# Optimization experiments

Measured on AMD Instinct MI355X. Metric: run time of the kernel, lower is better.

## Reference

```python
import jax
import jax.numpy as jnp
from jax import lax
import numpy as np

INPUT_DIM = 784
HIDDEN_DIM = 1024
BATCH = 256
N_BINS = 10


def setup_inputs() -> dict:
    key = jax.random.key(0)
    k1, k2, k3, k4, k5 = jax.random.split(key, 5)
    # kaiming-normal-ish init scales (faithful in spirit; exact values irrelevant for math)
    W = jax.random.normal(k1, (HIDDEN_DIM, INPUT_DIM), dtype=jnp.float32) * np.sqrt(2.0 / INPUT_DIM)
    c = jnp.zeros((HIDDEN_DIM, 1), dtype=jnp.float32)
    V = jax.random.normal(k2, (INPUT_DIM, HIDDEN_DIM, N_BINS), dtype=jnp.float32) * np.sqrt(2.0 / N_BINS)
    b = jnp.zeros((INPUT_DIM, N_BINS), dtype=jnp.float32)
    x = jax.random.randint(k3, (BATCH, INPUT_DIM), 0, N_BINS, dtype=jnp.int32)
    return {"x": x, "W": W, "c": c, "V": V, "b": b}


def reference(x, W, c, V, b):
    # x: [B, D] int pixel bins; W: [H, D]; c: [H, 1]; V: [D, H, 10]; b: [D, 10]
    B = x.shape[0]
    xf = x.astype(jnp.float32)  # [B, D]
    a0 = jnp.broadcast_to(c[:, 0][None, :], (B, W.shape[0]))  # [B, H]

    def step(a, inp):
        Vi, bi, Wi, xi = inp  # Vi:[H,10], bi:[10], Wi:[H], xi:[B]
        h = jax.nn.sigmoid(a)                       # [B, H]
        p = jax.nn.softmax(h @ Vi + bi, axis=1)     # [B, 10]
        a = a + xi[:, None] * Wi[None, :]           # rank-1 update, matches x_i @ W[:,i].T
        return a, p

    _, p_seq = lax.scan(step, a0, (V, b, W.T, xf.T))  # p_seq: [D, B, 10]
    p_hat = jnp.transpose(p_seq, (1, 2, 0))            # [B, 10, D] == torch.stack(p_hat, dim=2)
    return p_hat
```

## Files before the change

kernel.cpp:

```cpp
#include <hip/hip_runtime.h>
#include <stdint.h>

#define D_DIM 784
#define H_DIM 1024
#define B_DIM 256
#define NBIN  10
#define G_CH  8
#define T_CH  98
#define BT    16
#define BF    2
#define LOG2E 1.4426950408889634f

typedef _Float16 half8_t  __attribute__((ext_vector_type(8)));
typedef __fp16   fp16x2_t __attribute__((ext_vector_type(2)));
typedef float    float4_t __attribute__((ext_vector_type(4)));

__global__ void k_transpose(const float* __restrict__ W, float* __restrict__ Wt2) {
    __shared__ float t[64][65];
    int j0 = blockIdx.x * 64, h0 = blockIdx.y * 64;
    int tj = threadIdx.x & 63, tr = threadIdx.x >> 6;
    int j = j0 + tj;
    #pragma unroll
    for (int r = 0; r < 16; ++r) {
        int hh = tr * 16 + r;
        t[hh][tj] = (j < D_DIM) ? W[(size_t)(h0 + hh) * D_DIM + j] : 0.0f;
    }
    __syncthreads();
    #pragma unroll
    for (int r = 0; r < 16; ++r) {
        int jj = tr * 16 + r;
        int jo = j0 + jj;
        if (jo < D_DIM) Wt2[(size_t)jo * H_DIM + h0 + tj] = t[tj][jj] * LOG2E;
    }
}

__global__ void k_vbprep(const float* __restrict__ V, _Float16* __restrict__ VB) {
    int i   = blockIdx.x;
    int tid = threadIdx.x;
    __shared__ __align__(16) float vsf[H_DIM * NBIN];
    const float4* src = (const float4*)(V + (size_t)i * H_DIM * NBIN);
    #pragma unroll
    for (int q = 0; q < 10; ++q) {
        float4 v = src[q * 256 + tid];
        *((float4*)&vsf[(q * 256 + tid) * 4]) = v;
    }
    __syncthreads();
    #pragma unroll
    for (int q = 0; q < 8; ++q) {
        int pair = q * 256 + tid;
        int kk = pair >> 6, l = pair & 63;
        int n = l & 15, hb = kk * 32 + ((l >> 4) & 3) * 8;
        union { _Float16 h[8]; uint4 u; } o;
        #pragma unroll
        for (int jj = 0; jj < 8; ++jj)
            o.h[jj] = (_Float16)((n < NBIN) ? vsf[(hb + jj) * NBIN + n] : 0.0f);
        ((uint4*)VB)[(size_t)i * 2048 + pair] = o.u;
    }
}

__global__ void k_pscan(const float* __restrict__ Wt2, const int* __restrict__ x,
                        const float* __restrict__ c, _Float16* __restrict__ PA) {
    int b0 = blockIdx.x * BF;
    int h  = blockIdx.y * 256 + threadIdx.x;
    __shared__ float xs[BF][D_DIM];
    for (int q = threadIdx.x; q < BF * (D_DIM / 4); q += 256) {
        int bb = q / (D_DIM / 4), r = q % (D_DIM / 4);
        int4 xi = ((const int4*)(x + (size_t)(b0 + bb) * D_DIM))[r];
        float4 xf = make_float4((float)xi.x, (float)xi.y, (float)xi.z, (float)xi.w);
        *((float4*)&xs[bb][r * 4]) = xf;
    }
    float acc0 = c[h] * LOG2E, acc1 = acc0;
    __syncthreads();
    for (int t = 0; t < T_CH; ++t) {
        PA[((size_t)t * B_DIM + b0 + 0) * H_DIM + h] = (_Float16)acc0;
        PA[((size_t)t * B_DIM + b0 + 1) * H_DIM + h] = (_Float16)acc1;
        #pragma unroll
        for (int j = 0; j < G_CH; ++j) {
            float wv = Wt2[(size_t)(t * G_CH + j) * H_DIM + h];
            acc0 += xs[0][t * G_CH + j] * wv;
            acc1 += xs[1][t * G_CH + j] * wv;
        }
    }
}

__global__ __launch_bounds__(256, 2)
void k_main(const float* __restrict__ Wt2, const _Float16* __restrict__ VB,
            const _Float16* __restrict__ PA, const int* __restrict__ x,
            const float* __restrict__ bias, float* __restrict__ out) {
    int bt  = blockIdx.x;
    int tc  = blockIdx.y;
    int tid = threadIdx.x;
    int w   = tid >> 6;
    int l   = tid & 63;
    int bl  = l & 15;
    int kg  = l >> 4;
    int bg  = bt * BT + bl;
    int i0  = tc * G_CH;

    __shared__ __align__(16) _Float16 wlds[G_CH][H_DIM];
    __shared__ float red[2][4][64][5];
    __shared__ float bs[G_CH][16];
    __shared__ __align__(16) float plds[BT][NBIN][12];

    {
        int ii = tid >> 4, n = tid & 15;
        if (ii < G_CH) bs[ii][n] = (n < NBIN) ? bias[(size_t)(i0 + ii) * NBIN + n] : 0.0f;
    }
    {
        #pragma unroll
        for (int r = 0; r < G_CH; ++r) {
            float4 v = ((const float4*)(Wt2 + (size_t)(i0 + r) * H_DIM))[tid];
            union { fp16x2_t v2[2]; uint2 u; } cv;
            cv.v2[0] = __builtin_amdgcn_cvt_pkrtz(v.x, v.y);
            cv.v2[1] = __builtin_amdgcn_cvt_pkrtz(v.z, v.w);
            *((uint2*)&wlds[r][tid * 4]) = cv.u;
        }
    }
    float xvf[G_CH];
    {
        const int4* xp = (const int4*)(x + (size_t)bg * D_DIM + i0);
        int4 x0 = xp[0], x1 = xp[1];
        xvf[0] = (float)x0.x; xvf[1] = (float)x0.y; xvf[2] = (float)x0.z; xvf[3] = (float)x0.w;
        xvf[4] = (float)x1.x; xvf[5] = (float)x1.y; xvf[6] = (float)x1.z; xvf[7] = (float)x1.w;
    }
    float a[8][8];
    {
        const _Float16* src = PA + ((size_t)tc * B_DIM + bg) * H_DIM + w * 256 + kg * 8;
        #pragma unroll
        for (int m = 0; m < 8; ++m) {
            half8_t av = *((const half8_t*)(src + m * 32));
            #pragma unroll
            for (int j = 0; j < 8; ++j) a[m][j] = (float)av[j];
        }
    }
    __syncthreads();

    const uint4* vbbase = (const uint4*)VB;
    #pragma unroll 1
    for (int ii = 0; ii < G_CH; ++ii) {
        int i = i0 + ii;
        int par = ii & 1;

        uint4 vb[8];
        const uint4* vbp = vbbase + ((size_t)i * 32 + w * 8) * 64 + l;
        #pragma unroll
        for (int m = 0; m < 8; ++m) vb[m] = vbp[m * 64];

        if (ii > 0) {
            int ip = ii - 1, pp = par ^ 1;
            float tot = red[pp][0][l][w] + red[pp][1][l][w] + red[pp][2][l][w] + red[pp][3][l][w];
            int n = bl;
            float v = (n < NBIN) ? tot + bs[ip][n] : -3.0e38f;
            float vm = v;
            vm = fmaxf(vm, __shfl_xor(vm, 1));
            vm = fmaxf(vm, __shfl_xor(vm, 2));
            vm = fmaxf(vm, __shfl_xor(vm, 4));
            vm = fmaxf(vm, __shfl_xor(vm, 8));
            float e = __builtin_amdgcn_exp2f((v - vm) * LOG2E);
            float ss = e;
            ss += __shfl_xor(ss, 1); ss += __shfl_xor(ss, 2);
            ss += __shfl_xor(ss, 4); ss += __shfl_xor(ss, 8);
            float p = e * __builtin_amdgcn_rcpf(ss);
            if (n < NBIN) plds[kg * 4 + w][n][ip] = p;
        }

        float xf = xvf[ii];
        float4_t cfrag = {0.f, 0.f, 0.f, 0.f};
        #pragma unroll
        for (int m = 0; m < 8; ++m) {
            union { half8_t h8; uint u32[4]; } af;
            #pragma unroll
            for (int p = 0; p < 4; ++p) {
                float s0 = __builtin_amdgcn_rcpf(1.0f + __builtin_amdgcn_exp2f(-a[m][2 * p]));
                float s1 = __builtin_amdgcn_rcpf(1.0f + __builtin_amdgcn_exp2f(-a[m][2 * p + 1]));
                union { fp16x2_t v; uint u; } cv;
                cv.v = __builtin_amdgcn_cvt_pkrtz(s0, s1);
                af.u32[p] = cv.u;
            }
            union { half8_t h8; uint4 u; } bf;
            bf.u = vb[m];
            cfrag = __builtin_amdgcn_mfma_f32_16x16x32_f16(af.h8, bf.h8, cfrag, 0, 0, 0);

            half8_t wh = *((const half8_t*)&wlds[ii][w * 256 + kg * 8 + m * 32]);
            a[m][0] += xf * (float)wh[0]; a[m][1] += xf * (float)wh[1];
            a[m][2] += xf * (float)wh[2]; a[m][3] += xf * (float)wh[3];
            a[m][4] += xf * (float)wh[4]; a[m][5] += xf * (float)wh[5];
            a[m][6] += xf * (float)wh[6]; a[m][7] += xf * (float)wh[7];
        }

        red[par][w][l][0] = cfrag[0]; red[par][w][l][1] = cfrag[1];
        red[par][w][l][2] = cfrag[2]; red[par][w][l][3] = cfrag[3];
        __syncthreads();
    }
    {
        int ip = G_CH - 1, pp = (G_CH - 1) & 1;
        float tot = red[pp][0][l][w] + red[pp][1][l][w] + red[pp][2][l][w] + red[pp][3][l][w];
        int n = bl;
        float v = (n < NBIN) ? tot + bs[ip][n] : -3.0e38f;
        float vm = v;
        vm = fmaxf(vm, __shfl_xor(vm, 1));
        vm = fmaxf(vm, __shfl_xor(vm, 2));
        vm = fmaxf(vm, __shfl_xor(vm, 4));
        vm = fmaxf(vm, __shfl_xor(vm, 8));
        float e = __builtin_amdgcn_exp2f((v - vm) * LOG2E);
        float ss = e;
        ss += __shfl_xor(ss, 1); ss += __shfl_xor(ss, 2);
        ss += __shfl_xor(ss, 4); ss += __shfl_xor(ss, 8);
        float p = e * __builtin_amdgcn_rcpf(ss);
        if (n < NBIN) plds[kg * 4 + w][n][ip] = p;
    }
    __syncthreads();

    if (tid < BT * NBIN) {
        int bb = tid / NBIN, n = tid % NBIN;
        size_t base = ((size_t)(bt * BT + bb) * NBIN + n) * D_DIM + i0;
        #pragma unroll
        for (int q = 0; q < 2; ++q) {
            float4 v = *((float4*)&plds[bb][n][q * 4]);
            *((float4*)(out + base + q * 4)) = v;
        }
    }
}

extern "C" void kernel_launch(void* const* d_in, const int* in_sizes, int n_in,
                              void* d_out, int out_size, void* d_ws, size_t ws_size,
                              hipStream_t stream) {
    const int*   x    = (const int*)d_in[0];
    const float* W    = (const float*)d_in[1];
    const float* c    = (const float*)d_in[2];
    const float* V    = (const float*)d_in[3];
    const float* bias = (const float*)d_in[4];
    float* out = (float*)d_out;

    char* ws = (char*)d_ws;
    size_t off = 0;
    float* Wt2 = (float*)(ws + off);
    off += (size_t)D_DIM * H_DIM * sizeof(float);
    off = (off + 255) & ~(size_t)255;
    _Float16* VB = (_Float16*)(ws + off);
    off += (size_t)D_DIM * 32 * 64 * 8 * sizeof(_Float16);
    off = (off + 255) & ~(size_t)255;
    _Float16* PA = (_Float16*)(ws + off);

    k_transpose<<<dim3(13, 16), 256, 0, stream>>>(W, Wt2);
    k_vbprep<<<dim3(D_DIM), 256, 0, stream>>>(V, VB);
    k_pscan<<<dim3(B_DIM / BF, 4), 256, 0, stream>>>(Wt2, x, c, PA);
    k_main<<<dim3(B_DIM / BT, T_CH), 256, 0, stream>>>(Wt2, VB, PA, x, bias, out);
}
```

Measured before the change: 202.1 us.

## Merge prep kernels, store transposed W in fp16, batch softmax reductions in main

Fuses the W transpose and V reformat into one launch with a block-index split, and stores the scaled transposed W as fp16, which halves its traffic in pscan and main and removes the conversion in main. In the main kernel, per-step barriers and softmax are replaced by computing four pixel steps at a time, staging all four MFMA fragments into a wider LDS buffer, and doing softmax plus a direct float4 global store twice per block instead of eight times through a staging array. This cuts barriers from eight to four and removes the final output-staging pass. The cost is more live registers for the held fragments and lower-precision W in the prefix scan, whose errors accumulate across 784 steps.

```diff
diff --git a/kernel.cpp b/kernel.cpp
--- a/kernel.cpp
+++ b/kernel.cpp
@@ -15,50 +15,52 @@
 typedef __fp16   fp16x2_t __attribute__((ext_vector_type(2)));
 typedef float    float4_t __attribute__((ext_vector_type(4)));
 
-__global__ void k_transpose(const float* __restrict__ W, float* __restrict__ Wt2) {
-    __shared__ float t[64][65];
-    int j0 = blockIdx.x * 64, h0 = blockIdx.y * 64;
-    int tj = threadIdx.x & 63, tr = threadIdx.x >> 6;
-    int j = j0 + tj;
-    #pragma unroll
-    for (int r = 0; r < 16; ++r) {
-        int hh = tr * 16 + r;
-        t[hh][tj] = (j < D_DIM) ? W[(size_t)(h0 + hh) * D_DIM + j] : 0.0f;
-    }
-    __syncthreads();
-    #pragma unroll
-    for (int r = 0; r < 16; ++r) {
-        int jj = tr * 16 + r;
-        int jo = j0 + jj;
-        if (jo < D_DIM) Wt2[(size_t)jo * H_DIM + h0 + tj] = t[tj][jj] * LOG2E;
-    }
-}
-
-__global__ void k_vbprep(const float* __restrict__ V, _Float16* __restrict__ VB) {
-    int i   = blockIdx.x;
+__global__ void k_prep(const float* __restrict__ W, const float* __restrict__ V,
+                       _Float16* __restrict__ Wt2h, _Float16* __restrict__ VB) {
+    __shared__ __align__(16) float smem[H_DIM * NBIN];
     int tid = threadIdx.x;
-    __shared__ __align__(16) float vsf[H_DIM * NBIN];
-    const float4* src = (const float4*)(V + (size_t)i * H_DIM * NBIN);
-    #pragma unroll
-    for (int q = 0; q < 10; ++q) {
-        float4 v = src[q * 256 + tid];
-        *((float4*)&vsf[(q * 256 + tid) * 4]) = v;
-    }
-    __syncthreads();
-    #pragma unroll
-    for (int q = 0; q < 8; ++q) {
-        int pair = q * 256 + tid;
-        int kk = pair >> 6, l = pair & 63;
-        int n = l & 15, hb = kk * 32 + ((l >> 4) & 3) * 8;
-        union { _Float16 h[8]; uint4 u; } o;
-        #pragma unroll
-        for (int jj = 0; jj < 8; ++jj)
-            o.h[jj] = (_Float16)((n < NBIN) ? vsf[(hb + jj) * NBIN + n] : 0.0f);
-        ((uint4*)VB)[(size_t)i * 2048 + pair] = o.u;
-    }
-}
-
-__global__ void k_pscan(const float* __restrict__ Wt2, const int* __restrict__ x,
+    if (blockIdx.x < D_DIM) {
+        int i = blockIdx.x;
+        const float4* src = (const float4*)(V + (size_t)i * H_DIM * NBIN);
+        #pragma unroll
+        for (int q = 0; q < 10; ++q) {
+            float4 v = src[q * 256 + tid];
+            *((float4*)&smem[(q * 256 + tid) * 4]) = v;
+        }
+        __syncthreads();
+        #pragma unroll
+        for (int q = 0; q < 8; ++q) {
+            int pair = q * 256 + tid;
+            int kk = pair >> 6, l = pair & 63;
+            int n = l & 15, hb = kk * 32 + ((l >> 4) & 3) * 8;
+            union { _Float16 h[8]; uint4 u; } o;
+            #pragma unroll
+            for (int jj = 0; jj < 8; ++jj)
+                o.h[jj] = (_Float16)((n < NBIN) ? smem[(hb + jj) * NBIN + n] : 0.0f);
+            ((uint4*)VB)[(size_t)i * 2048 + pair] = o.u;
+        }
+    } else {
+        int q = blockIdx.x - D_DIM;
+        int j0 = (q % 13) * 64, h0 = (q / 13) * 64;
+        float (*t)[65] = (float(*)[65])smem;
+        int tj = tid & 63, tr = tid >> 6;
+        int j = j0 + tj;
+        #pragma unroll
+        for (int r = 0; r < 16; ++r) {
+            int hh = tr * 16 + r;
+            t[hh][tj] = (j < D_DIM) ? W[(size_t)(h0 + hh) * D_DIM + j] : 0.0f;
+        }
+        __syncthreads();
+        #pragma unroll
+        for (int r = 0; r < 16; ++r) {
+            int jj = tr * 16 + r;
+            int jo = j0 + jj;
+            if (jo < D_DIM) Wt2h[(size_t)jo * H_DIM + h0 + tj] = (_Float16)(t[tj][jj] * LOG2E);
+        }
+    }
+}
+
+__global__ void k_pscan(const _Float16* __restrict__ Wt2h, const int* __restrict__ x,
                         const float* __restrict__ c, _Float16* __restrict__ PA) {
     int b0 = blockIdx.x * BF;
     int h  = blockIdx.y * 256 + threadIdx.x;
@@ -76,7 +78,7 @@
         PA[((size_t)t * B_DIM + b0 + 1) * H_DIM + h] = (_Float16)acc1;
         #pragma unroll
         for (int j = 0; j < G_CH; ++j) {
-            float wv = Wt2[(size_t)(t * G_CH + j) * H_DIM + h];
+            float wv = (float)Wt2h[(size_t)(t * G_CH + j) * H_DIM + h];
             acc0 += xs[0][t * G_CH + j] * wv;
             acc1 += xs[1][t * G_CH + j] * wv;
         }
@@ -84,7 +86,7 @@
 }
 
 __global__ __launch_bounds__(256, 2)
-void k_main(const float* __restrict__ Wt2, const _Float16* __restrict__ VB,
+void k_main(const _Float16* __restrict__ VB, const _Float16* __restrict__ Wt2h,
             const _Float16* __restrict__ PA, const int* __restrict__ x,
             const float* __restrict__ bias, float* __restrict__ out) {
     int bt  = blockIdx.x;
@@ -98,9 +100,8 @@
     int i0  = tc * G_CH;
 
     __shared__ __align__(16) _Float16 wlds[G_CH][H_DIM];
-    __shared__ float red[2][4][64][5];
+    __shared__ float red[4][64][18];
     __shared__ float bs[G_CH][16];
-    __shared__ __align__(16) float plds[BT][NBIN][12];
 
     {
         int ii = tid >> 4, n = tid & 15;
@@ -109,11 +110,8 @@
     {
         #pragma unroll
         for (int r = 0; r < G_CH; ++r) {
-            float4 v = ((const float4*)(Wt2 + (size_t)(i0 + r) * H_DIM))[tid];
-            union { fp16x2_t v2[2]; uint2 u; } cv;
-            cv.v2[0] = __builtin_amdgcn_cvt_pkrtz(v.x, v.y);
-            cv.v2[1] = __builtin_amdgcn_cvt_pkrtz(v.z, v.w);
-            *((uint2*)&wlds[r][tid * 4]) = cv.u;
+            uint2 v = ((const uint2*)(Wt2h + (size_t)(i0 + r) * H_DIM))[tid];
+            *((uint2*)&wlds[r][tid * 4]) = v;
         }
     }
     float xvf[G_CH];
@@ -136,36 +134,16 @@
     __syncthreads();
 
     const uint4* vbbase = (const uint4*)VB;
-    #pragma unroll 1
-    for (int ii = 0; ii < G_CH; ++ii) {
+    float4_t cf[G_CH];
+
+    auto compute_ii = [&](int ii) {
         int i = i0 + ii;
-        int par = ii & 1;
-
         uint4 vb[8];
         const uint4* vbp = vbbase + ((size_t)i * 32 + w * 8) * 64 + l;
         #pragma unroll
         for (int m = 0; m < 8; ++m) vb[m] = vbp[m * 64];
-
-        if (ii > 0) {
-            int ip = ii - 1, pp = par ^ 1;
-            float tot = red[pp][0][l][w] + red[pp][1][l][w] + red[pp][2][l][w] + red[pp][3][l][w];
-            int n = bl;
-            float v = (n < NBIN) ? tot + bs[ip][n] : -3.0e38f;
-            float vm = v;
-            vm = fmaxf(vm, __shfl_xor(vm, 1));
-            vm = fmaxf(vm, __shfl_xor(vm, 2));
-            vm = fmaxf(vm, __shfl_xor(vm, 4));
-            vm = fmaxf(vm, __shfl_xor(vm, 8));
-            float e = __builtin_amdgcn_exp2f((v - vm) * LOG2E);
-            float ss = e;
-            ss += __shfl_xor(ss, 1); ss += __shfl_xor(ss, 2);
-            ss += __shfl_xor(ss, 4); ss += __shfl_xor(ss, 8);
-            float p = e * __builtin_amdgcn_rcpf(ss);
-            if (n < NBIN) plds[kg * 4 + w][n][ip] = p;
-        }
-
         float xf = xvf[ii];
-        float4_t cfrag = {0.f, 0.f, 0.f, 0.f};
+        float4_t cfr = {0.f, 0.f, 0.f, 0.f};
         #pragma unroll
         for (int m = 0; m < 8; ++m) {
             union { half8_t h8; uint u32[4]; } af;
@@ -179,47 +157,60 @@
             }
             union { half8_t h8; uint4 u; } bf;
             bf.u = vb[m];
-            cfrag = __builtin_amdgcn_mfma_f32_16x16x32_f16(af.h8, bf.h8, cfrag, 0, 0, 0);
-
+            cfr = __builtin_amdgcn_mfma_f32_16x16x32_f16(af.h8, bf.h8, cfr, 0, 0, 0);
             half8_t wh = *((const half8_t*)&wlds[ii][w * 256 + kg * 8 + m * 32]);
             a[m][0] += xf * (float)wh[0]; a[m][1] += xf * (float)wh[1];
             a[m][2] += xf * (float)wh[2]; a[m][3] += xf * (float)wh[3];
             a[m][4] += xf * (float)wh[4]; a[m][5] += xf * (float)wh[5];
             a[m][6] += xf * (float)wh[6]; a[m][7] += xf * (float)wh[7];
         }
-
-        red[par][w][l][0] = cfrag[0]; red[par][w][l][1] = cfrag[1];
-        red[par][w][l][2] = cfrag[2]; red[par][w][l][3] = cfrag[3];
-        __syncthreads();
-    }
-    {
-        int ip = G_CH - 1, pp = (G_CH - 1) & 1;
-        float tot = red[pp][0][l][w] + red[pp][1][l][w] + red[pp][2][l][w] + red[pp][3][l][w];
-        int n = bl;
-        float v = (n < NBIN) ? tot + bs[ip][n] : -3.0e38f;
-        float vm = v;
-        vm = fmaxf(vm, __shfl_xor(vm, 1));
-        vm = fmaxf(vm, __shfl_xor(vm, 2));
-        vm = fmaxf(vm, __shfl_xor(vm, 4));
-        vm = fmaxf(vm, __shfl_xor(vm, 8));
-        float e = __builtin_amdgcn_exp2f((v - vm) * LOG2E);
-        float ss = e;
-        ss += __shfl_xor(ss, 1); ss += __shfl_xor(ss, 2);
-        ss += __shfl_xor(ss, 4); ss += __shfl_xor(ss, 8);
-        float p = e * __builtin_amdgcn_rcpf(ss);
-        if (n < NBIN) plds[kg * 4 + w][n][ip] = p;
-    }
-    __syncthreads();
-
-    if (tid < BT * NBIN) {
-        int bb = tid / NBIN, n = tid % NBIN;
-        size_t base = ((size_t)(bt * BT + bb) * NBIN + n) * D_DIM + i0;
-        #pragma unroll
-        for (int q = 0; q < 2; ++q) {
-            float4 v = *((float4*)&plds[bb][n][q * 4]);
-            *((float4*)(out + base + q * 4)) = v;
-        }
-    }
+        cf[ii] = cfr;
+    };
+
+    auto softmax_store = [&](int half) {
+        float p4[4];
+        #pragma unroll
+        for (int q = 0; q < 4; ++q) {
+            int ii = half * 4 + q;
+            float tot = red[0][l][q * 4 + w] + red[1][l][q * 4 + w]
+                      + red[2][l][q * 4 + w] + red[3][l][q * 4 + w];
+            float v = (bl < NBIN) ? tot + bs[ii][bl] : -3.0e38f;
+            float vm = v;
+            vm = fmaxf(vm, __shfl_xor(vm, 1));
+            vm = fmaxf(vm, __shfl_xor(vm, 2));
+            vm = fmaxf(vm, __shfl_xor(vm, 4));
+            vm = fmaxf(vm, __shfl_xor(vm, 8));
+            float e = __builtin_amdgcn_exp2f((v - vm) * LOG2E);
+            float ss = e;
+            ss += __shfl_xor(ss, 1); ss += __shfl_xor(ss, 2);
+            ss += __shfl_xor(ss, 4); ss += __shfl_xor(ss, 8);
+            p4[q] = e * __builtin_amdgcn_rcpf(ss);
+        }
+        if (bl < NBIN) {
+            int b = bt * BT + kg * 4 + w;
+            size_t base = ((size_t)b * NBIN + bl) * D_DIM + i0 + half * 4;
+            float4 v = make_float4(p4[0], p4[1], p4[2], p4[3]);
+            *((float4*)(out + base)) = v;
+        }
+    };
+
+    for (int q = 0; q < 4; ++q) compute_ii(q);
+    #pragma unroll
+    for (int q = 0; q < 4; ++q) {
+        #pragma unroll
+        for (int r = 0; r < 4; ++r) red[w][l][q * 4 + r] = cf[q][r];
+    }
+    __syncthreads();
+    for (int q = 0; q < 4; ++q) compute_ii(4 + q);
+    softmax_store(0);
+    __syncthreads();
+    #pragma unroll
+    for (int q = 0; q < 4; ++q) {
+        #pragma unroll
+        for (int r = 0; r < 4; ++r) red[w][l][q * 4 + r] = cf[4 + q][r];
+    }
+    __syncthreads();
+    softmax_store(1);
 }
 
 extern "C" void kernel_launch(void* const* d_in, const int* in_sizes, int n_in,
@@ -234,16 +225,15 @@
 
     char* ws = (char*)d_ws;
     size_t off = 0;
-    float* Wt2 = (float*)(ws + off);
-    off += (size_t)D_DIM * H_DIM * sizeof(float);
+    _Float16* Wt2h = (_Float16*)(ws + off);
+    off += (size_t)D_DIM * H_DIM * sizeof(_Float16);
     off = (off + 255) & ~(size_t)255;
     _Float16* VB = (_Float16*)(ws + off);
     off += (size_t)D_DIM * 32 * 64 * 8 * sizeof(_Float16);
     off = (off + 255) & ~(size_t)255;
     _Float16* PA = (_Float16*)(ws + off);
 
-    k_transpose<<<dim3(13, 16), 256, 0, stream>>>(W, Wt2);
-    k_vbprep<<<dim3(D_DIM), 256, 0, stream>>>(V, VB);
-    k_pscan<<<dim3(B_DIM / BF, 4), 256, 0, stream>>>(Wt2, x, c, PA);
-    k_main<<<dim3(B_DIM / BT, T_CH), 256, 0, stream>>>(Wt2, VB, PA, x, bias, out);
-}
+    k_prep<<<dim3(D_DIM + 208), 256, 0, stream>>>(W, V, Wt2h, VB);
+    k_pscan<<<dim3(B_DIM / BF, 4), 256, 0, stream>>>(Wt2h, x, c, PA);
+    k_main<<<dim3(B_DIM / BT, T_CH), 256, 0, stream>>>(VB, Wt2h, PA, x, bias, out);
+}
```

Result: faster. 187.7 us (-7.1%).
